# Kernel optimization log

Hardware: AMD Instinct MI355X
Metric: run time of the kernel (lower is better)

Reference implementation:

```python
import jax, jax.numpy as jnp
import numpy as np

K = 3      # kernel_size
PAD = 1    # (dilation*(K-1)+1)//2 with dilation=1
EPS = 1e-3 # keras BatchNormalization default epsilon


def _unfold(x, k=K, pad=PAD):
    # reflect-pad local-window gather, torch.nn.functional.unfold ordering
    # x: [N,C,H,W] -> [N,C,k*k,H*W]
    N, C, H, W = x.shape
    xp = jnp.pad(x, ((0, 0), (0, 0), (pad, pad), (pad, pad)), mode='reflect')
    pats = jnp.stack([xp[:, :, i:i + H, j:j + W] for i in range(k) for j in range(k)], axis=2)
    return pats.reshape(N, C, k * k, H * W)


def _position(H, W):
    # [1,2,H,W]: channel 0 = x(-1..1 across W), channel 1 = y(-1..1 across H)
    loc_w = jnp.tile(jnp.linspace(-1.0, 1.0, W)[None, :], (H, 1))
    loc_h = jnp.tile(jnp.linspace(-1.0, 1.0, H)[:, None], (1, W))
    return jnp.stack([loc_w, loc_h], axis=0)[None].astype(jnp.float32)


def _bn(x, g, b, m, v):
    # keras BN, default axis=-1 (here the H*W axis), inference mode
    return (x - m) / jnp.sqrt(v + EPS) * g + b


def setup_inputs():
    key = jax.random.key(0)
    ks = jax.random.split(key, 16)
    N, C, H, W = 16, 256, 56, 56
    REL, OUT, SHARE = 16, 64, 8
    HW = H * W
    f = lambda k_, s: jax.random.normal(k_, s, dtype=jnp.float32)
    return {
        'x': f(ks[0], (N, C, H, W)),
        'conv1_w': f(ks[1], (REL, C)) * 0.05,
        'conv2_w': f(ks[2], (REL, C)) * 0.05,
        'conv3_w': f(ks[3], (OUT, C)) * 0.05,
        'convp_w': f(ks[4], (2, 2)),
        'convw1_w': f(ks[5], (REL, REL + 2)) * 0.2,
        'convw2_w': f(ks[6], (OUT // SHARE, REL)) * 0.2,
        'bn1_gamma': 1.0 + 0.1 * f(ks[7], (HW,)),
        'bn1_beta': 0.1 * f(ks[8], (HW,)),
        'bn1_mean': 0.1 * f(ks[9], (HW,)),
        'bn1_var': 1.0 + 0.5 * jax.random.uniform(ks[10], (HW,), dtype=jnp.float32),
        'bn2_gamma': 1.0 + 0.1 * f(ks[11], (HW,)),
        'bn2_beta': 0.1 * f(ks[12], (HW,)),
        'bn2_mean': 0.1 * f(ks[13], (HW,)),
        'bn2_var': 1.0 + 0.5 * jax.random.uniform(ks[14], (HW,), dtype=jnp.float32),
    }


def reference(x, conv1_w, conv2_w, conv3_w, convp_w, convw1_w, convw2_w,
              bn1_gamma, bn1_beta, bn1_mean, bn1_var,
              bn2_gamma, bn2_beta, bn2_mean, bn2_var):
    N, C, H, W = x.shape
    HW = H * W
    # 1x1 convs (channels_first) as channel contractions
    x1 = jnp.einsum('oc,nchw->nohw', conv1_w, x)
    x2 = jnp.einsum('oc,nchw->nohw', conv2_w, x)
    x3 = jnp.einsum('oc,nchw->nohw', conv3_w, x)
    p = jnp.einsum('oc,nchw->nohw', convp_w, _position(H, W))  # [1,2,H,W]
    # subtraction2(x1, x2): center feature minus windowed neighbors -> [N,rel,k^2,HW]
    sub2 = x1.reshape(N, -1, 1, HW) - _unfold(x2)
    # subtraction(p): relative positions -> [1,2,k^2,HW], tiled over batch
    subp = p.reshape(1, 2, 1, HW) - _unfold(p)
    rel = jnp.concatenate([sub2, jnp.tile(subp, (N, 1, 1, 1))], axis=1)  # [N,rel+2,k^2,HW]
    # conv_w: BN -> ReLU -> 1x1 conv -> BN -> ReLU -> 1x1 conv
    h = jax.nn.relu(_bn(rel, bn1_gamma, bn1_beta, bn1_mean, bn1_var))
    h = jnp.einsum('oc,ncjl->nojl', convw1_w, h)
    h = jax.nn.relu(_bn(h, bn2_gamma, bn2_beta, bn2_mean, bn2_var))
    h = jnp.einsum('oc,ncjl->nojl', convw2_w, h)  # [N,out//share,k^2,HW]
    w = jax.nn.softmax(h, axis=-2)                # softmax over the k^2 window axis
    # aggregation: weighted neighbor sum, weight channel shared by share_planes channels
    xu = _unfold(x3)                              # [N,out,k^2,HW]
    c_w = w.shape[1]
    xu = xu.reshape(N, -1, c_w, K * K, HW)        # channel c -> (c//c_w, c%c_w)
    out = jnp.einsum('ncjl,ngcjl->ngcl', w, xu)   # sum over window positions j
    return out.reshape(N, -1, H, W)
```

## Files before the change

kernel.cpp:

```cpp
#include <hip/hip_runtime.h>

typedef short bf16x8 __attribute__((ext_vector_type(8)));
typedef float floatx4 __attribute__((ext_vector_type(4)));
typedef unsigned short ushort4v __attribute__((ext_vector_type(4)));
typedef unsigned int uintx4 __attribute__((ext_vector_type(4)));
typedef unsigned int uintx2 __attribute__((ext_vector_type(2)));

#define HW 3136
#define WS 100

#define P_CP   0
#define P_W1   4
#define P_W2   292
#define P_BN   424
#define PREP_FLOATS (424 + 4 * HW)

__device__ __forceinline__ unsigned short f2bf(float f) {
    unsigned int u = __float_as_uint(f);
    unsigned int r = (u + 0x7FFFu + ((u >> 16) & 1u)) >> 16;
    return (unsigned short)r;
}
__device__ __forceinline__ float bf2f(unsigned short u) {
    return __uint_as_float(((unsigned int)u) << 16);
}
__device__ __forceinline__ void unp8(uint4 u, float* o) {
    o[0] = bf2f((unsigned short)(u.x & 0xFFFFu)); o[1] = bf2f((unsigned short)(u.x >> 16));
    o[2] = bf2f((unsigned short)(u.y & 0xFFFFu)); o[3] = bf2f((unsigned short)(u.y >> 16));
    o[4] = bf2f((unsigned short)(u.z & 0xFFFFu)); o[5] = bf2f((unsigned short)(u.z >> 16));
    o[6] = bf2f((unsigned short)(u.w & 0xFFFFu)); o[7] = bf2f((unsigned short)(u.w >> 16));
}
__device__ __forceinline__ float ldp(const void* p, int i, int isb) {
    return isb ? bf2f(((const unsigned short*)p)[i]) : ((const float*)p)[i];
}

struct __align__(16) Stage { unsigned int b[16]; bf16x8 a; };

template <int ISB>
__device__ __forceinline__ void ldstage(const void* x, size_t xb,
                                        const void* wp, int arow, int ch, Stage& s)
{
    if (ISB) {
        const unsigned short* p = (const unsigned short*)x + xb + (size_t)ch * HW;
        #pragma unroll
        for (int j = 0; j < 8; ++j)
            *(uintx2*)&s.b[2 * j] = *(const uintx2*)(p + (size_t)j * HW);
        s.a = *(const bf16x8*)((const unsigned short*)wp + arow * 256 + ch);
    } else {
        const float* p = (const float*)x + xb + (size_t)ch * HW;
        #pragma unroll
        for (int j = 0; j < 8; ++j) {
            floatx4 f = *(const floatx4*)(p + (size_t)j * HW);
            s.b[2 * j + 0] = (unsigned)f2bf(f[0]) | ((unsigned)f2bf(f[1]) << 16);
            s.b[2 * j + 1] = (unsigned)f2bf(f[2]) | ((unsigned)f2bf(f[3]) << 16);
        }
        const float* fp = (const float*)wp + arow * 256 + ch;
        bf16x8 a;
        #pragma unroll
        for (int j = 0; j < 8; ++j) a[j] = (short)f2bf(fp[j]);
        s.a = a;
    }
}

__device__ __forceinline__ void domfma(const Stage& s, floatx4 (&acc)[4])
{
    #pragma unroll
    for (int t = 0; t < 4; ++t) {
        const int wi = t >> 1;
        uintx4 uv;
        #pragma unroll
        for (int d = 0; d < 4; ++d) {
            const unsigned lo = s.b[2 * (2 * d) + wi];
            const unsigned hi = s.b[2 * (2 * d + 1) + wi];
            const unsigned v = (t & 1) ? ((lo >> 16) | (hi & 0xFFFF0000u))
                                       : ((lo & 0xFFFFu) | (hi << 16));
            uv[d] = v;
        }
        bf16x8 B = __builtin_bit_cast(bf16x8, uv);
        acc[t] = __builtin_amdgcn_mfma_f32_16x16x32_bf16(s.a, B, acc[t], 0, 0, 0);
    }
}

template <int ISB>
__device__ void proj_body(const void* x, const void* wp, int arow,
                          size_t xb, int quad, floatx4 (&acc)[4])
{
    Stage s0, s1;
    ldstage<ISB>(x, xb, wp, arow, quad * 8, s0);
    #pragma unroll
    for (int q = 0; q < 8; q += 2) {
        ldstage<ISB>(x, xb, wp, arow, (q + 1) * 32 + quad * 8, s1);
        domfma(s0, acc);
        if (q + 2 < 8)
            ldstage<ISB>(x, xb, wp, arow, (q + 2) * 32 + quad * 8, s0);
        domfma(s1, acc);
    }
}

template <int ISB>
__global__ __launch_bounds__(384, 3) void proj_kernel(
    const void* __restrict__ x,
    const void* __restrict__ w1, const void* __restrict__ w2,
    const void* __restrict__ w3,
    const void* __restrict__ cpw, const void* __restrict__ cw1,
    const void* __restrict__ cw2,
    const void* __restrict__ b1g, const void* __restrict__ b1b,
    const void* __restrict__ b1m, const void* __restrict__ b1v,
    const void* __restrict__ b2g, const void* __restrict__ b2b,
    const void* __restrict__ b2m, const void* __restrict__ b2v,
    unsigned short* __restrict__ y12,
    unsigned short* __restrict__ y3a,
    float* __restrict__ prep)
{
    const int tid = threadIdx.x;

    if (blockIdx.x < 16) {
        if (blockIdx.x == 0) {
            for (int i = tid; i < 420; i += 384) {
                float v;
                if      (i < 4)   v = ldp(cpw, i,        ISB);
                else if (i < 292) v = ldp(cw1, i - 4,    ISB);
                else              v = ldp(cw2, i - 292,  ISB);
                prep[i] = v;
            }
        }
        const int i0 = blockIdx.x * 196;
        if (tid < 196) {
            const int i = i0 + tid;
            float a1 = ldp(b1g, i, ISB) * rsqrtf(ldp(b1v, i, ISB) + 1e-3f);
            float c1 = ldp(b1b, i, ISB) - ldp(b1m, i, ISB) * a1;
            float a2 = ldp(b2g, i, ISB) * rsqrtf(ldp(b2v, i, ISB) + 1e-3f);
            float c2 = ldp(b2b, i, ISB) - ldp(b2m, i, ISB) * a2;
            prep[P_BN + i]          = a1;
            prep[P_BN + HW + i]     = c1;
            prep[P_BN + 2 * HW + i] = a2;
            prep[P_BN + 3 * HW + i] = c2;
        }
    }

    const int n   = blockIdx.x / 49;
    const int pt  = blockIdx.x - n * 49;
    const int px0 = pt * 64;
    const int rt  = tid >> 6;
    const int lane = tid & 63;
    const int col = lane & 15, quad = lane >> 4;

    const void* wp; int ro;
    if      (rt == 0) { wp = w1; ro = 0;  }
    else if (rt == 1) { wp = w2; ro = 0;  }
    else if (rt == 2) { wp = w3; ro = 0;  }
    else if (rt == 3) { wp = w3; ro = 16; }
    else if (rt == 4) { wp = w3; ro = 32; }
    else              { wp = w3; ro = 48; }

    const size_t xb = (size_t)n * 256 * HW + px0 + 4 * col;

    floatx4 acc[4] = {};
    proj_body<ISB>(x, wp, ro + col, xb, quad, acc);

    const int chq = quad * 4;
    #pragma unroll
    for (int tt = 0; tt < 4; ++tt) {
        const int px = px0 + 4 * col + tt;
        ushort4v pk;
        #pragma unroll
        for (int g = 0; g < 4; ++g) pk[g] = f2bf(acc[tt][g]);
        if (rt < 2) {
            *(ushort4v*)(y12 + ((size_t)n * HW + px) * 32 + rt * 16 + chq) = pk;
        } else {
            const int k8 = 2 * (rt - 2) + (quad >> 1);
            *(ushort4v*)(y3a + (((size_t)n * 8 + k8) * HW + px) * 8 + (quad & 1) * 4) = pk;
        }
    }
}

template <int ISB>
__global__ __launch_bounds__(576, 8) void attn_kernel(
    const unsigned short* __restrict__ y12,
    const unsigned short* __restrict__ y3a,
    const float* __restrict__ prep,
    void* __restrict__ out)
{
    __shared__ float wsm[64 * WS];
    const int tid = threadIdx.x;
    const int blk = blockIdx.x;
    const int n   = blk / 49;
    const int l0  = (blk - n * 49) * 64;

    {
        const int j = tid >> 6;
        const int p = tid & 63;
        const int l = l0 + p;
        const int h = l / 56, w = l - h * 56;
        const int dy = j / 3 - 1, dx = j - (j / 3) * 3 - 1;
        int hh = h + dy; hh = (hh < 0) ? -hh : ((hh > 55) ? 110 - hh : hh);
        int ww = w + dx; ww = (ww < 0) ? -ww : ((ww > 55) ? 110 - ww : ww);
        const int nbr = hh * 56 + ww;

        const float a1 = prep[P_BN + l];
        const float c1 = prep[P_BN + HW + l];
        const float a2 = prep[P_BN + 2 * HW + l];
        const float c2 = prep[P_BN + 3 * HW + l];

        const unsigned short* y1p = y12 + ((size_t)n * HW + l) * 32;
        const unsigned short* y2p = y12 + ((size_t)n * HW + nbr) * 32 + 16;

        float rel[18];
        #pragma unroll
        for (int half = 0; half < 2; ++half) {
            uint4 u1 = *(const uint4*)(y1p + 8 * half);
            uint4 u2 = *(const uint4*)(y2p + 8 * half);
            float t1[8], t2[8];
            unp8(u1, t1);
            unp8(u2, t2);
            #pragma unroll
            for (int c = 0; c < 8; ++c)
                rel[8 * half + c] = fmaxf(fmaf(t1[c] - t2[c], a1, c1), 0.f);
        }
        const float dlw = (float)(w - ww) * (2.0f / 55.0f);
        const float dlh = (float)(h - hh) * (2.0f / 55.0f);
        rel[16] = fmaxf(fmaf(prep[P_CP + 0] * dlw + prep[P_CP + 1] * dlh, a1, c1), 0.f);
        rel[17] = fmaxf(fmaf(prep[P_CP + 2] * dlw + prep[P_CP + 3] * dlh, a1, c1), 0.f);

        float h1[16];
        #pragma unroll
        for (int o = 0; o < 16; ++o) {
            float s = 0.f;
            #pragma unroll
            for (int c = 0; c < 18; ++c)
                s = fmaf(prep[P_W1 + o * 18 + c], rel[c], s);
            h1[o] = fmaxf(fmaf(s, a2, c2), 0.f);
        }
        float h2[8];
        #pragma unroll
        for (int o2 = 0; o2 < 8; ++o2) {
            float s = 0.f;
            #pragma unroll
            for (int o = 0; o < 16; ++o)
                s = fmaf(prep[P_W2 + o2 * 16 + o], h1[o], s);
            h2[o2] = s;
        }
        float* wpt = &wsm[p * WS + j * 8];
        *(floatx4*)wpt       = *(floatx4*)&h2[0];
        *(floatx4*)(wpt + 4) = *(floatx4*)&h2[4];
    }
    __syncthreads();

    if (tid < 512) {
        const int c = tid & 7, p = tid >> 3;
        float v[9];
        #pragma unroll
        for (int j = 0; j < 9; ++j) v[j] = wsm[p * WS + j * 8 + c];
        float m = v[0];
        #pragma unroll
        for (int j = 1; j < 9; ++j) m = fmaxf(m, v[j]);
        float s = 0.f;
        #pragma unroll
        for (int j = 0; j < 9; ++j) { v[j] = __expf(v[j] - m); s += v[j]; }
        const float inv = 1.f / s;
        #pragma unroll
        for (int j = 0; j < 9; ++j) wsm[p * WS + j * 8 + c] = v[j] * inv;
    }
    __syncthreads();

    if (tid < 512) {
        const int p  = tid & 63;
        const int k8 = tid >> 6;
        const int l = l0 + p;
        const int h = l / 56, w = l - h * 56;
        int nbr[9];
        #pragma unroll
        for (int dy = 0; dy < 3; ++dy)
            #pragma unroll
            for (int dx = 0; dx < 3; ++dx) {
                int hh = h + dy - 1; hh = (hh < 0) ? -hh : ((hh > 55) ? 110 - hh : hh);
                int ww = w + dx - 1; ww = (ww < 0) ? -ww : ((ww > 55) ? 110 - ww : ww);
                nbr[dy * 3 + dx] = hh * 56 + ww;
            }
        const unsigned short* y3b = y3a + ((size_t)n * 8 + k8) * HW * 8;
        float acc8[8];
        #pragma unroll
        for (int k = 0; k < 8; ++k) acc8[k] = 0.f;
        #pragma unroll
        for (int j = 0; j < 9; ++j) {
            uint4 u = *(const uint4*)(y3b + (size_t)nbr[j] * 8);
            float yv[8];
            unp8(u, yv);
            const float* wpt = &wsm[p * WS + j * 8];
            #pragma unroll
            for (int k = 0; k < 8; ++k)
                acc8[k] = fmaf(wpt[k], yv[k], acc8[k]);
        }
        const size_t obase = ((size_t)n * 64 + k8 * 8) * HW + l;
        #pragma unroll
        for (int k = 0; k < 8; ++k) {
            if (ISB) ((unsigned short*)out)[obase + (size_t)k * HW] = f2bf(acc8[k]);
            else     ((float*)out)[obase + (size_t)k * HW]          = acc8[k];
        }
    }
}

extern "C" void kernel_launch(void* const* d_in, const int* in_sizes, int n_in,
                              void* d_out, int out_size, void* d_ws, size_t ws_size,
                              hipStream_t stream)
{
    const size_t y12B = (size_t)16 * HW * 32 * 2;
    const size_t y3aB = (size_t)16 * 8 * HW * 8 * 2;

    unsigned short* y12 = (unsigned short*)d_ws;
    unsigned short* y3a = (unsigned short*)((char*)d_ws + y12B);
    float* prep = (float*)((char*)d_ws + y12B + y3aB);

    const int isb = (in_sizes[10] == HW * 2);

    if (isb) {
        proj_kernel<1><<<dim3(784), dim3(384), 0, stream>>>(
            d_in[0], d_in[1], d_in[2], d_in[3],
            d_in[4], d_in[5], d_in[6],
            d_in[7], d_in[8], d_in[9], d_in[10],
            d_in[11], d_in[12], d_in[13], d_in[14],
            y12, y3a, prep);
        attn_kernel<1><<<dim3(784), dim3(576), 0, stream>>>(y12, y3a, prep, d_out);
    } else {
        proj_kernel<0><<<dim3(784), dim3(384), 0, stream>>>(
            d_in[0], d_in[1], d_in[2], d_in[3],
            d_in[4], d_in[5], d_in[6],
            d_in[7], d_in[8], d_in[9], d_in[10],
            d_in[11], d_in[12], d_in[13], d_in[14],
            y12, y3a, prep);
        attn_kernel<0><<<dim3(784), dim3(576), 0, stream>>>(y12, y3a, prep, d_out);
    }
}
```

Baseline: 150.4 us.

## Share x tile across waves via LDS instead of per-wave redundant global loads

Before, each of the six waves in a block loaded and converted the full 256-channel slice of x for its 64-pixel tile. Now the waves split the 8 channel stages between them (waves 0-1 take two stages each), convert them to bf16 MFMA B-fragments once, and store them in LDS. After a barrier, every wave reads the fragments back and runs its MFMAs with the weight fragments preloaded into registers. This removes six-fold redundant global traffic and conversion work, at the cost of 32KB of LDS per block, a __syncthreads, and no more load/compute overlap. The occupancy hint is raised from 3 to 6 blocks per CU.

```diff
diff --git a/kernel.cpp b/kernel.cpp
--- a/kernel.cpp
+++ b/kernel.cpp
@@ -33,71 +33,43 @@
     return isb ? bf2f(((const unsigned short*)p)[i]) : ((const float*)p)[i];
 }
 
-struct __align__(16) Stage { unsigned int b[16]; bf16x8 a; };
-
 template <int ISB>
-__device__ __forceinline__ void ldstage(const void* x, size_t xb,
-                                        const void* wp, int arow, int ch, Stage& s)
+__device__ __forceinline__ void stage_one(const void* x, size_t xpx, int s,
+                                          int quad, int lane, uintx4* frag)
 {
+    const int ch0 = s * 32 + quad * 8;
+    unsigned b[16];
     if (ISB) {
-        const unsigned short* p = (const unsigned short*)x + xb + (size_t)ch * HW;
+        const unsigned short* p = (const unsigned short*)x + xpx + (size_t)ch0 * HW;
         #pragma unroll
         for (int j = 0; j < 8; ++j)
-            *(uintx2*)&s.b[2 * j] = *(const uintx2*)(p + (size_t)j * HW);
-        s.a = *(const bf16x8*)((const unsigned short*)wp + arow * 256 + ch);
+            *(uintx2*)&b[2 * j] = *(const uintx2*)(p + (size_t)j * HW);
     } else {
-        const float* p = (const float*)x + xb + (size_t)ch * HW;
+        const float* p = (const float*)x + xpx + (size_t)ch0 * HW;
         #pragma unroll
         for (int j = 0; j < 8; ++j) {
             floatx4 f = *(const floatx4*)(p + (size_t)j * HW);
-            s.b[2 * j + 0] = (unsigned)f2bf(f[0]) | ((unsigned)f2bf(f[1]) << 16);
-            s.b[2 * j + 1] = (unsigned)f2bf(f[2]) | ((unsigned)f2bf(f[3]) << 16);
-        }
-        const float* fp = (const float*)wp + arow * 256 + ch;
-        bf16x8 a;
-        #pragma unroll
-        for (int j = 0; j < 8; ++j) a[j] = (short)f2bf(fp[j]);
-        s.a = a;
-    }
-}
-
-__device__ __forceinline__ void domfma(const Stage& s, floatx4 (&acc)[4])
-{
+            b[2 * j]     = (unsigned)f2bf(f[0]) | ((unsigned)f2bf(f[1]) << 16);
+            b[2 * j + 1] = (unsigned)f2bf(f[2]) | ((unsigned)f2bf(f[3]) << 16);
+        }
+    }
     #pragma unroll
     for (int t = 0; t < 4; ++t) {
         const int wi = t >> 1;
         uintx4 uv;
         #pragma unroll
         for (int d = 0; d < 4; ++d) {
-            const unsigned lo = s.b[2 * (2 * d) + wi];
-            const unsigned hi = s.b[2 * (2 * d + 1) + wi];
-            const unsigned v = (t & 1) ? ((lo >> 16) | (hi & 0xFFFF0000u))
-                                       : ((lo & 0xFFFFu) | (hi << 16));
-            uv[d] = v;
-        }
-        bf16x8 B = __builtin_bit_cast(bf16x8, uv);
-        acc[t] = __builtin_amdgcn_mfma_f32_16x16x32_bf16(s.a, B, acc[t], 0, 0, 0);
+            const unsigned lo = b[2 * (2 * d) + wi];
+            const unsigned hi = b[2 * (2 * d + 1) + wi];
+            uv[d] = (t & 1) ? ((lo >> 16) | (hi & 0xFFFF0000u))
+                            : ((lo & 0xFFFFu) | (hi << 16));
+        }
+        frag[(s * 4 + t) * 64 + lane] = uv;
     }
 }
 
 template <int ISB>
-__device__ void proj_body(const void* x, const void* wp, int arow,
-                          size_t xb, int quad, floatx4 (&acc)[4])
-{
-    Stage s0, s1;
-    ldstage<ISB>(x, xb, wp, arow, quad * 8, s0);
-    #pragma unroll
-    for (int q = 0; q < 8; q += 2) {
-        ldstage<ISB>(x, xb, wp, arow, (q + 1) * 32 + quad * 8, s1);
-        domfma(s0, acc);
-        if (q + 2 < 8)
-            ldstage<ISB>(x, xb, wp, arow, (q + 2) * 32 + quad * 8, s0);
-        domfma(s1, acc);
-    }
-}
-
-template <int ISB>
-__global__ __launch_bounds__(384, 3) void proj_kernel(
+__global__ __launch_bounds__(384, 6) void proj_kernel(
     const void* __restrict__ x,
     const void* __restrict__ w1, const void* __restrict__ w2,
     const void* __restrict__ w3,
@@ -111,6 +83,7 @@
     unsigned short* __restrict__ y3a,
     float* __restrict__ prep)
 {
+    __shared__ uintx4 frag[8 * 4 * 64];
     const int tid = threadIdx.x;
 
     if (blockIdx.x < 16) {
@@ -137,12 +110,17 @@
         }
     }
 
-    const int n   = blockIdx.x / 49;
-    const int pt  = blockIdx.x - n * 49;
-    const int px0 = pt * 64;
-    const int rt  = tid >> 6;
+    const int n    = blockIdx.x / 49;
+    const int pt   = blockIdx.x - n * 49;
+    const int px0  = pt * 64;
+    const int rt   = tid >> 6;
     const int lane = tid & 63;
-    const int col = lane & 15, quad = lane >> 4;
+    const int col  = lane & 15, quad = lane >> 4;
+
+    const size_t xpx = (size_t)n * 256 * HW + px0 + 4 * col;
+
+    stage_one<ISB>(x, xpx, rt, quad, lane, frag);
+    if (rt < 2) stage_one<ISB>(x, xpx, 6 + rt, quad, lane, frag);
 
     const void* wp; int ro;
     if      (rt == 0) { wp = w1; ro = 0;  }
@@ -151,11 +129,44 @@
     else if (rt == 3) { wp = w3; ro = 16; }
     else if (rt == 4) { wp = w3; ro = 32; }
     else              { wp = w3; ro = 48; }
-
-    const size_t xb = (size_t)n * 256 * HW + px0 + 4 * col;
+    const int arow = ro + col;
+
+    bf16x8 a[8];
+    if (ISB) {
+        const unsigned short* fp = (const unsigned short*)wp + arow * 256 + quad * 8;
+        #pragma unroll
+        for (int s = 0; s < 8; ++s)
+            a[s] = *(const bf16x8*)(fp + s * 32);
+    } else {
+        const float* fp = (const float*)wp + arow * 256 + quad * 8;
+        #pragma unroll
+        for (int s = 0; s < 8; ++s) {
+            floatx4 f0 = *(const floatx4*)(fp + s * 32);
+            floatx4 f1 = *(const floatx4*)(fp + s * 32 + 4);
+            bf16x8 av;
+            #pragma unroll
+            for (int j = 0; j < 4; ++j) {
+                av[j]     = (short)f2bf(f0[j]);
+                av[4 + j] = (short)f2bf(f1[j]);
+            }
+            a[s] = av;
+        }
+    }
+
+    __syncthreads();
 
     floatx4 acc[4] = {};
-    proj_body<ISB>(x, wp, ro + col, xb, quad, acc);
+    #pragma unroll
+    for (int s = 0; s < 8; ++s) {
+        uintx4 f[4];
+        #pragma unroll
+        for (int t = 0; t < 4; ++t)
+            f[t] = frag[(s * 4 + t) * 64 + lane];
+        #pragma unroll
+        for (int t = 0; t < 4; ++t)
+            acc[t] = __builtin_amdgcn_mfma_f32_16x16x32_bf16(
+                a[s], __builtin_bit_cast(bf16x8, f[t]), acc[t], 0, 0, 0);
+    }
 
     const int chq = quad * 4;
     #pragma unroll
```

Result: faster. 142.1 us (-5.5%).
